# Kernel tuning notes

Measured on AMD Instinct MI355X. Metric: run time of the kernel, lower is better.

Reference implementation:

```python
import jax, jax.numpy as jnp
import numpy as np

N_NODES = 100000
N_EDGES = 3200000  # avg degree 32
IN_FEATS = 512
N_HIDDEN = 128
N_CLASSES = 64
K = 10  # n_layers of gated APPNP propagation


def setup_inputs() -> dict:
    key = jax.random.key(0)
    ks = jax.random.split(key, 6)
    features = jax.random.normal(ks[0], (N_NODES, IN_FEATS), dtype=jnp.float32)
    W1 = jax.random.normal(ks[1], (IN_FEATS, N_HIDDEN), dtype=jnp.float32) * (1.0 / np.sqrt(IN_FEATS))
    b1 = jnp.zeros((N_HIDDEN,), jnp.float32)
    W2 = jax.random.normal(ks[2], (N_HIDDEN, N_CLASSES), dtype=jnp.float32) * (1.0 / np.sqrt(N_HIDDEN))
    b2 = jnp.zeros((N_CLASSES,), jnp.float32)
    init_weight_y = jax.random.normal(ks[3], (IN_FEATS, N_CLASSES), dtype=jnp.float32) * (1.0 / np.sqrt(IN_FEATS))
    edge_index = jax.random.randint(ks[4], (2, N_EDGES), 0, N_NODES, dtype=jnp.int32)
    return {
        "features": features, "W1": W1, "b1": b1, "W2": W2, "b2": b2,
        "init_weight_y": init_weight_y, "edge_index": edge_index,
    }


def reference(features, W1, b1, W2, b2, init_weight_y, edge_index):
    # Eval-mode forward: feat/edge dropout are identity.
    src, dst = edge_index[0], edge_index[1]
    n = features.shape[0]
    # Symmetric GCN normalization D^{-1/2} A D^{-1/2} from in-degrees.
    deg = jax.ops.segment_sum(jnp.ones(src.shape, features.dtype), dst, num_segments=n)
    norm = jax.lax.rsqrt(jnp.clip(deg, 1.0))
    ew = (norm[src] * norm[dst])[:, None]  # [E,1] edge weights

    def spmm(x):  # A_hat @ x via gather-multiply-scatter
        return jax.ops.segment_sum(x[src] * ew, dst, num_segments=n)

    # feature transform: dropout(identity) -> linear -> relu
    h = jax.nn.relu(features @ W1 + b1)                      # [N,H]
    logits = jax.nn.softmax(features @ init_weight_y, axis=1)  # [N,C]
    # project predictions before propagation (APPNP propagates class scores)
    h0 = h @ W2 + b2                                         # [N,C]

    def step(carry, _):
        hc, lg = carry
        agg_lg = spmm(lg)                                    # neighbor soft labels
        # gate: per-node agreement between own and aggregated soft labels
        z = jax.nn.sigmoid(jnp.sum(lg * agg_lg, axis=1, keepdims=True))  # [N,1]
        h_new = z * spmm(hc) + (1.0 - z) * h0                # gated APPNP hop
        return (h_new, agg_lg), None

    (h_out, _), _ = jax.lax.scan(step, (h0, logits), None, length=K)
    return h_out
```

## Files before the change

### kernel.cpp

```cpp
#include <hip/hip_runtime.h>

typedef __attribute__((ext_vector_type(8))) short bf16x8;
typedef __attribute__((ext_vector_type(4))) short bf16x4;
typedef __attribute__((ext_vector_type(4))) float f32x4;
typedef __attribute__((ext_vector_type(4))) unsigned int u32x4;

__device__ __forceinline__ unsigned short f2bf(float f) {
  unsigned int u = __float_as_uint(f);
  u += 0x7fffu + ((u >> 16) & 1u);
  return (unsigned short)(u >> 16);
}
__device__ __forceinline__ float bflo(unsigned int w) { return __uint_as_float(w << 16); }
__device__ __forceinline__ float bfhi(unsigned int w) { return __uint_as_float(w & 0xffff0000u); }

__device__ __forceinline__ unsigned e8(float f) {
  unsigned u = __float_as_uint(f) + (1u << 19);
  int cd = (int)(u >> 20) - 920;
  cd = cd < 0 ? 0 : (cd > 255 ? 255 : cd);
  return (unsigned)cd;
}
__device__ __forceinline__ float d8(unsigned code) {
  return __uint_as_float((code << 20) + (115u << 23));
}

__device__ __forceinline__ short* ldsp(short* base, int row, int rowbytes, int colshort) {
  int off = row * rowbytes + colshort * 2;
  off ^= ((row & 7) << 4);
  return (short*)((char*)base + off);
}

#define CHUNK 8192
#define NBMAX 512
#define BCAP 12288
#define DCAP 96

__global__ __launch_bounds__(256) void k_bucket(const int* __restrict__ ei,
                                                int* __restrict__ gcur,
                                                int2* __restrict__ bpairs, int E, int NB) {
  __shared__ int lhist[NBMAX];
  __shared__ int lbase[NBMAX];
  __shared__ int lcur[NBMAX];
  for (int t = threadIdx.x; t < NB; t += 256) lhist[t] = 0;
  __syncthreads();
  int base = blockIdx.x * CHUNK;
#pragma unroll
  for (int i = 0; i < CHUNK / 256; ++i) {
    int e = base + i * 256 + threadIdx.x;
    if (e < E) atomicAdd(&lhist[ei[E + e] >> 8], 1);
  }
  __syncthreads();
  for (int t = threadIdx.x; t < NB; t += 256) {
    int c = lhist[t];
    lbase[t] = c ? atomicAdd(&gcur[t], c) : 0;
    lcur[t] = 0;
  }
  __syncthreads();
#pragma unroll
  for (int i = 0; i < CHUNK / 256; ++i) {
    int e = base + i * 256 + threadIdx.x;
    if (e < E) {
      int s = ei[e], d = ei[E + e];
      int b = d >> 8;
      int p = lbase[b] + atomicAdd(&lcur[b], 1);
      bpairs[(size_t)b * BCAP + p] = make_int2(s, d);
    }
  }
}

__global__ __launch_bounds__(256) void k_csr(const int2* __restrict__ bpairs,
                                             const int* __restrict__ bcnt,
                                             int* __restrict__ offs, int* __restrict__ deg,
                                             float* __restrict__ nrm,
                                             int* __restrict__ csr_src,
                                             int* __restrict__ gslots, int N) {
  __shared__ int hist[256];
  __shared__ int scan[256];
  __shared__ int cur[256];
  const int t = threadIdx.x;
  const int b = blockIdx.x;
  const int d0 = b << 8;
  const int nn = min(256, N - d0);
  const int base = b * BCAP;
  const int end = base + bcnt[b];
  hist[t] = 0;
  __syncthreads();
  for (int e = base + t; e < end; e += 256) atomicAdd(&hist[bpairs[e].y - d0], 1);
  __syncthreads();
  int myc = hist[t];
  scan[t] = myc;
  __syncthreads();
  for (int o = 1; o < 256; o <<= 1) {
    int x = (t >= o) ? scan[t - o] : 0;
    __syncthreads();
    scan[t] += x;
    __syncthreads();
  }
  int excl = scan[t] - myc;
  if (t < nn) {
    offs[d0 + t] = base + excl;
    deg[d0 + t] = myc;
    nrm[d0 + t] = rsqrtf(fmaxf((float)myc, 1.f));
  }
  if (t < 64) {
    int w0 = hist[4 * t + 0], w1 = hist[4 * t + 1];
    int w2 = hist[4 * t + 2], w3 = hist[4 * t + 3];
    gslots[b * 64 + t] = 4 * max(max(w0, w1), max(w2, w3));
  }
  cur[t] = excl;
  __syncthreads();
  for (int e = base + t; e < end; e += 256) {
    int2 pr = bpairs[e];
    int pos = atomicAdd(&cur[pr.y - d0], 1);
    csr_src[base + pos] = pr.x;
  }
}

__global__ void k_scan1(const int* __restrict__ in, int* __restrict__ out,
                        int* __restrict__ bsum, int n) {
  __shared__ int sm[1024];
  int t = threadIdx.x;
  int gid = blockIdx.x * 1024 + t;
  int v = (gid < n) ? in[gid] : 0;
  sm[t] = v;
  __syncthreads();
  for (int off = 1; off < 1024; off <<= 1) {
    int x = (t >= off) ? sm[t - off] : 0;
    __syncthreads();
    sm[t] += x;
    __syncthreads();
  }
  if (gid < n) out[gid] = sm[t] - v;
  if (t == 1023) bsum[blockIdx.x] = sm[1023];
}

__global__ void k_scan2(int* __restrict__ bsum, int nb) {
  __shared__ int sm[128];
  int t = threadIdx.x;
  int v = (t < nb) ? bsum[t] : 0;
  sm[t] = v;
  __syncthreads();
  for (int o = 1; o < 128; o <<= 1) {
    int x = (t >= o) ? sm[t - o] : 0;
    __syncthreads();
    sm[t] += x;
    __syncthreads();
  }
  if (t < nb) bsum[t] = sm[t] - v;
  if (t == 127) bsum[nb] = sm[127];
}

__global__ void k_scan3(int* __restrict__ out, const int* __restrict__ bsum, int n) {
  int gid = blockIdx.x * 1024 + threadIdx.x;
  if (gid < n) out[gid] += bsum[blockIdx.x];
  if (gid == 0) out[n] = bsum[gridDim.x];
}

__global__ __launch_bounds__(64) void k_ell(
    const int* __restrict__ offs, const int* __restrict__ deg,
    const int* __restrict__ csr_src,
    const int* __restrict__ gof, unsigned* __restrict__ pidx,
    unsigned* __restrict__ HA, unsigned* __restrict__ HB,
    unsigned* __restrict__ LA, unsigned* __restrict__ LB, int N) {
  __shared__ int buf[4][DCAP];
  __shared__ int srt[4][DCAP];
  int g = blockIdx.x;
  int t = threadIdx.x;
  if (g == 0) {
    if (t < 32) { HA[(size_t)N * 32 + t] = 0; HB[(size_t)N * 32 + t] = 0; }
    if (t < 16) { LA[(size_t)N * 16 + t] = 0; LB[(size_t)N * 16 + t] = 0; }
  }
  int base = gof[g];
  int slots = gof[g + 1] - base;
  int o[4], d[4];
#pragma unroll
  for (int s = 0; s < 4; ++s) {
    int nd_ = g * 4 + s;
    o[s] = (nd_ < N) ? offs[nd_] : 0;
    d[s] = (nd_ < N) ? deg[nd_] : 0;
  }
  const int ls = t >> 4;
  const int ll = t & 15;
  const int dd = d[ls];
  const bool srtable = (dd <= DCAP);
  if (srtable)
    for (int i = ll; i < dd; i += 16) buf[ls][i] = csr_src[o[ls] + i];
  __syncthreads();
  if (srtable) {
    for (int i = ll; i < dd; i += 16) {
      int key = buf[ls][i];
      int r = 0;
      for (int j = 0; j < dd; ++j) {
        int v = buf[ls][j];
        r += (v < key) || (v == key && j < i);
      }
      srt[ls][r] = key;
    }
  }
  __syncthreads();
  unsigned zoff = (unsigned)N << 6;
  for (int j = t; j < slots; j += 64) {
    int i = j >> 2, s = j & 3;
    unsigned v = zoff;
    if (i < d[s]) v = (unsigned)((d[s] <= DCAP) ? srt[s][i] : csr_src[o[s] + i]) << 6;
    pidx[base + j] = v;
  }
}

__global__ void k_wprep(const float* __restrict__ W1, const float* __restrict__ Wy,
                        unsigned short* __restrict__ Wt) {
  int k = blockIdx.x, j = threadIdx.x;
  float v = (j < 128) ? W1[k * 128 + j] : Wy[k * 64 + (j - 128)];
  Wt[j * 512 + k] = f2bf(v);
}
__global__ void k_wprep2(const float* __restrict__ W2, unsigned short* __restrict__ Wt2) {
  int k = blockIdx.x, j = threadIdx.x;
  Wt2[j * 128 + k] = f2bf(W2[k * 64 + j]);
}

__global__ __launch_bounds__(256) void k_transform(
    const unsigned short* __restrict__ Wt, const unsigned short* __restrict__ Wt2,
    const float* __restrict__ X, const float* __restrict__ b1, const float* __restrict__ b2,
    const float* __restrict__ nrm,
    unsigned* __restrict__ Hrow0, unsigned* __restrict__ Lrow0,
    unsigned short* __restrict__ h0b, int n)
{
  __shared__ short Xs[128 * 32];
  __shared__ short Ws[192 * 32];
  __shared__ short Hs[128 * 128];
  __shared__ short W2s[64 * 128];

  const int tid = threadIdx.x;
  const int w = tid >> 6;
  const int lane = tid & 63;
  const int c = lane & 15;
  const int g = lane >> 4;
  const int m0 = blockIdx.x * 128;

#pragma unroll
  for (int i = 0; i < 4; ++i) {
    int cc = tid + i * 256;
    int j2 = cc >> 4, k8 = (cc & 15) * 8;
    bf16x8 v = *(const bf16x8*)&Wt2[j2 * 128 + k8];
    *(bf16x8*)ldsp(W2s, j2, 256, k8) = v;
  }

  f32x4 zero4 = {0.f, 0.f, 0.f, 0.f};
  f32x4 acc[2][12];
#pragma unroll
  for (int mi = 0; mi < 2; ++mi)
#pragma unroll
    for (int i = 0; i < 12; ++i) acc[mi][i] = zero4;

  const int xr = tid >> 1;
  const int xc = (tid & 1) * 16;
  const int xrow = m0 + xr;

  for (int kk = 0; kk < 512; kk += 32) {
    float4 f[4];
    if (xrow < n) {
      const float4* p = (const float4*)(X + (size_t)xrow * 512 + kk + xc);
      f[0] = p[0]; f[1] = p[1]; f[2] = p[2]; f[3] = p[3];
    } else {
      float4 z = {0.f, 0.f, 0.f, 0.f};
      f[0] = z; f[1] = z; f[2] = z; f[3] = z;
    }
    {
      const float* fp = (const float*)f;
      unsigned p0, p1, p2, p3, q0, q1, q2, q3;
      asm("v_cvt_pk_bf16_f32 %0, %1, %2" : "=v"(p0) : "v"(fp[0]),  "v"(fp[1]));
      asm("v_cvt_pk_bf16_f32 %0, %1, %2" : "=v"(p1) : "v"(fp[2]),  "v"(fp[3]));
      asm("v_cvt_pk_bf16_f32 %0, %1, %2" : "=v"(p2) : "v"(fp[4]),  "v"(fp[5]));
      asm("v_cvt_pk_bf16_f32 %0, %1, %2" : "=v"(p3) : "v"(fp[6]),  "v"(fp[7]));
      asm("v_cvt_pk_bf16_f32 %0, %1, %2" : "=v"(q0) : "v"(fp[8]),  "v"(fp[9]));
      asm("v_cvt_pk_bf16_f32 %0, %1, %2" : "=v"(q1) : "v"(fp[10]), "v"(fp[11]));
      asm("v_cvt_pk_bf16_f32 %0, %1, %2" : "=v"(q2) : "v"(fp[12]), "v"(fp[13]));
      asm("v_cvt_pk_bf16_f32 %0, %1, %2" : "=v"(q3) : "v"(fp[14]), "v"(fp[15]));
      u32x4 lo = {p0, p1, p2, p3};
      u32x4 hi = {q0, q1, q2, q3};
      *(u32x4*)ldsp(Xs, xr, 64, xc) = lo;
      *(u32x4*)ldsp(Xs, xr, 64, xc + 8) = hi;
    }
#pragma unroll
    for (int i = 0; i < 3; ++i) {
      int cc = tid + i * 256;
      int j = cc >> 2, k8 = (cc & 3) * 8;
      bf16x8 v = *(const bf16x8*)&Wt[j * 512 + kk + k8];
      *(bf16x8*)ldsp(Ws, j, 64, k8) = v;
    }
    __syncthreads();
    bf16x8 bx0 = *(const bf16x8*)ldsp(Xs, w * 32 + c, 64, g * 8);
    bf16x8 bx1 = *(const bf16x8*)ldsp(Xs, w * 32 + 16 + c, 64, g * 8);
#pragma unroll
    for (int jt = 0; jt < 12; ++jt) {
      bf16x8 aw = *(const bf16x8*)ldsp(Ws, jt * 16 + c, 64, g * 8);
      acc[0][jt] = __builtin_amdgcn_mfma_f32_16x16x32_bf16(aw, bx0, acc[0][jt], 0, 0, 0);
      acc[1][jt] = __builtin_amdgcn_mfma_f32_16x16x32_bf16(aw, bx1, acc[1][jt], 0, 0, 0);
    }
    __syncthreads();
  }

  float lv[2][16];
  float inv_[2];
#pragma unroll
  for (int mi = 0; mi < 2; ++mi) {
    int m = w * 32 + mi * 16 + c;
#pragma unroll
    for (int jt = 0; jt < 8; ++jt) {
      int jb = jt * 16 + g * 4;
      bf16x4 hv;
#pragma unroll
      for (int q = 0; q < 4; ++q) {
        float hvf = fmaxf(acc[mi][jt][q] + b1[jb + q], 0.f);
        hv[q] = (short)f2bf(hvf);
      }
      *(bf16x4*)ldsp(Hs, m, 256, jb) = hv;
    }
    float mx = -3.4e38f;
#pragma unroll
    for (int t = 0; t < 4; ++t)
#pragma unroll
      for (int q = 0; q < 4; ++q) {
        float vv = acc[mi][8 + t][q];
        lv[mi][t * 4 + q] = vv;
        mx = fmaxf(mx, vv);
      }
    mx = fmaxf(mx, __shfl_xor(mx, 16, 64));
    mx = fmaxf(mx, __shfl_xor(mx, 32, 64));
    float sum = 0.f;
#pragma unroll
    for (int i = 0; i < 16; ++i) { lv[mi][i] = __expf(lv[mi][i] - mx); sum += lv[mi][i]; }
    sum += __shfl_xor(sum, 16, 64);
    sum += __shfl_xor(sum, 32, 64);
    inv_[mi] = 1.f / sum;
  }
  __syncthreads();

  f32x4 acc2[2][4];
#pragma unroll
  for (int mi = 0; mi < 2; ++mi)
#pragma unroll
    for (int i = 0; i < 4; ++i) acc2[mi][i] = zero4;
#pragma unroll
  for (int kk2 = 0; kk2 < 4; ++kk2) {
    bf16x8 bh0 = *(const bf16x8*)ldsp(Hs, w * 32 + c, 256, kk2 * 32 + g * 8);
    bf16x8 bh1 = *(const bf16x8*)ldsp(Hs, w * 32 + 16 + c, 256, kk2 * 32 + g * 8);
#pragma unroll
    for (int j2t = 0; j2t < 4; ++j2t) {
      bf16x8 a2 = *(const bf16x8*)ldsp(W2s, j2t * 16 + c, 256, kk2 * 32 + g * 8);
      acc2[0][j2t] = __builtin_amdgcn_mfma_f32_16x16x32_bf16(a2, bh0, acc2[0][j2t], 0, 0, 0);
      acc2[1][j2t] = __builtin_amdgcn_mfma_f32_16x16x32_bf16(a2, bh1, acc2[1][j2t], 0, 0, 0);
    }
  }

#pragma unroll
  for (int mi = 0; mi < 2; ++mi) {
    int m = w * 32 + mi * 16 + c;
    int grow = m0 + m;
    if (grow < n) {
      float nd = nrm[grow];
#pragma unroll
      for (int t = 0; t < 4; ++t) {
        int cb = t * 16 + g * 4;
        bf16x4 hb;
        unsigned short hs[4];
        unsigned lw = 0;
#pragma unroll
        for (int q = 0; q < 4; ++q) {
          float lg  = lv[mi][t * 4 + q] * inv_[mi];
          float h0v = acc2[mi][t][q] + b2[cb + q];
          hb[q]  = (short)f2bf(h0v);
          hs[q]  = f2bf(nd * h0v);
          lw |= e8(64.f * nd * lg) << (8 * q);
        }
        uint2 hw;
        hw.x = (unsigned)hs[0] | ((unsigned)hs[1] << 16);
        hw.y = (unsigned)hs[2] | ((unsigned)hs[3] << 16);
        *(uint2*)((char*)Hrow0 + (size_t)grow * 128 + cb * 2) = hw;
        *(unsigned*)((char*)Lrow0 + (size_t)grow * 64 + cb) = lw;
        *(bf16x4*)(h0b + (size_t)grow * 64 + cb) = hb;
      }
    }
  }
}

__global__ __launch_bounds__(256) void k_prop(
    const int* __restrict__ gof, const unsigned* __restrict__ pidx,
    const unsigned* __restrict__ Hin, const unsigned* __restrict__ Lin,
    unsigned* __restrict__ Hout, unsigned* __restrict__ Lout,
    const unsigned short* __restrict__ h0b, const float* __restrict__ nrm,
    float* __restrict__ final_out, int n, int ng, int last)
{
  const int lane = threadIdx.x & 63;
  const int g = blockIdx.x * 4 + (threadIdx.x >> 6);
  if (g >= ng) return;
  const int sub = lane >> 4;
  const int cq  = lane & 15;
  const int node = g * 4 + sub;
  const int beg = gof[g];
  const int w = (gof[g + 1] - beg) >> 2;
  const char* Hc = (const char*)Hin;
  const char* Lc = (const char*)Lin;
  const unsigned* ib = pidx + beg + sub;
  const int hco = cq << 3;
  const int lco = cq << 2;

  const int nodeC = (node < n) ? node : 0;
  unsigned ownl = *(const unsigned*)(Lc + ((size_t)nodeC << 6) + lco);
  float nd = nrm[nodeC];
  bf16x4 h0v = *(const bf16x4*)(h0b + (size_t)nodeC * 64 + cq * 4);

  float aH[4] = {0.f, 0.f, 0.f, 0.f}, aL[4] = {0.f, 0.f, 0.f, 0.f};
  float bH[4] = {0.f, 0.f, 0.f, 0.f}, bL[4] = {0.f, 0.f, 0.f, 0.f};
  int i = 0;
  for (; i + 4 <= w; i += 4) {
    unsigned x0 = ib[4 * i], x1 = ib[4 * i + 4], x2 = ib[4 * i + 8], x3 = ib[4 * i + 12];
    uint2 h0_ = *(const uint2*)(Hc + (((size_t)x0 << 1) + hco));
    uint2 h1_ = *(const uint2*)(Hc + (((size_t)x1 << 1) + hco));
    uint2 h2_ = *(const uint2*)(Hc + (((size_t)x2 << 1) + hco));
    uint2 h3_ = *(const uint2*)(Hc + (((size_t)x3 << 1) + hco));
    unsigned l0 = *(const unsigned*)(Lc + (x0 + lco));
    unsigned l1 = *(const unsigned*)(Lc + (x1 + lco));
    unsigned l2 = *(const unsigned*)(Lc + (x2 + lco));
    unsigned l3 = *(const unsigned*)(Lc + (x3 + lco));
    aH[0] += bflo(h0_.x) + bflo(h2_.x); aH[1] += bfhi(h0_.x) + bfhi(h2_.x);
    aH[2] += bflo(h0_.y) + bflo(h2_.y); aH[3] += bfhi(h0_.y) + bfhi(h2_.y);
    bH[0] += bflo(h1_.x) + bflo(h3_.x); bH[1] += bfhi(h1_.x) + bfhi(h3_.x);
    bH[2] += bflo(h1_.y) + bflo(h3_.y); bH[3] += bfhi(h1_.y) + bfhi(h3_.y);
#pragma unroll
    for (int q = 0; q < 4; ++q) {
      aL[q] += d8((l0 >> (8 * q)) & 255u) + d8((l2 >> (8 * q)) & 255u);
      bL[q] += d8((l1 >> (8 * q)) & 255u) + d8((l3 >> (8 * q)) & 255u);
    }
  }
  for (; i < w; ++i) {
    unsigned x0 = ib[4 * i];
    uint2 h0_ = *(const uint2*)(Hc + (((size_t)x0 << 1) + hco));
    unsigned l0 = *(const unsigned*)(Lc + (x0 + lco));
    aH[0] += bflo(h0_.x); aH[1] += bfhi(h0_.x);
    aH[2] += bflo(h0_.y); aH[3] += bfhi(h0_.y);
#pragma unroll
    for (int q = 0; q < 4; ++q) aL[q] += d8((l0 >> (8 * q)) & 255u);
  }
#pragma unroll
  for (int q = 0; q < 4; ++q) { aH[q] += bH[q]; aL[q] += bL[q]; }

  if (node >= n) return;
  float p = 0.f;
#pragma unroll
  for (int q = 0; q < 4; ++q) p += d8((ownl >> (8 * q)) & 255u) * aL[q];
  p += __shfl_xor(p, 1, 64);
  p += __shfl_xor(p, 2, 64);
  p += __shfl_xor(p, 4, 64);
  p += __shfl_xor(p, 8, 64);
  float z = 1.f / (1.f + __expf(-p * (1.f / 4096.f)));

  if (last) {
    float4 o;
    float* op = &o.x;
#pragma unroll
    for (int q = 0; q < 4; ++q) {
      float h0f = __uint_as_float(((unsigned)(unsigned short)h0v[q]) << 16);
      op[q] = z * nd * aH[q] + (1.f - z) * h0f;
    }
    *(float4*)(final_out + (size_t)node * 64 + cq * 4) = o;
  } else {
    float nn2 = nd * nd;
    unsigned short hs[4];
    unsigned lw = 0;
#pragma unroll
    for (int q = 0; q < 4; ++q) {
      float h0f = __uint_as_float(((unsigned)(unsigned short)h0v[q]) << 16);
      float hn = z * nd * aH[q] + (1.f - z) * h0f;
      hs[q] = f2bf(nd * hn);
      lw |= e8(nn2 * aL[q]) << (8 * q);
    }
    uint2 hw;
    hw.x = (unsigned)hs[0] | ((unsigned)hs[1] << 16);
    hw.y = (unsigned)hs[2] | ((unsigned)hs[3] << 16);
    *(uint2*)((char*)Hout + (((size_t)node << 7) + hco)) = hw;
    *(unsigned*)((char*)Lout + (((size_t)node << 6) + lco)) = lw;
  }
}

extern "C" void kernel_launch(void* const* d_in, const int* in_sizes, int n_in,
                              void* d_out, int out_size, void* d_ws, size_t ws_size,
                              hipStream_t stream) {
  (void)n_in; (void)out_size; (void)ws_size;
  const float* X  = (const float*)d_in[0];
  const float* W1 = (const float*)d_in[1];
  const float* b1 = (const float*)d_in[2];
  const float* W2 = (const float*)d_in[3];
  const float* b2 = (const float*)d_in[4];
  const float* Wy = (const float*)d_in[5];
  const int*   ei = (const int*)d_in[6];
  const int N = in_sizes[0] / 512;
  const int E = in_sizes[6] / 2;
  const int NB = (N + 255) >> 8;
  const int NG = NB * 64;
  const int NWG = (E + CHUNK - 1) / CHUNK;

  char* p = (char*)d_ws;
  auto alloc = [&](size_t bytes) -> char* {
    char* r = p; p += (bytes + 255) & ~(size_t)255; return r;
  };
  int*            gcur    = (int*)  alloc(NBMAX * 4);
  int*            offs    = (int*)  alloc((size_t)N * 4);
  int*            deg     = (int*)  alloc((size_t)N * 4);
  float*          nrm     = (float*)alloc((size_t)N * 4);
  int*            csr_src = (int*)  alloc((size_t)NB * BCAP * 4);
  int*            gslots  = (int*)  alloc((size_t)(NG + 1) * 4);
  int*            gof     = (int*)  alloc((size_t)(NG + 1) * 4);
  int*            sbsum   = (int*)  alloc(1024);
  unsigned*       pidx    = (unsigned*)alloc((size_t)2 * E * 4);
  unsigned short* Wt      = (unsigned short*)alloc(192 * 512 * 2);
  unsigned short* Wt2     = (unsigned short*)alloc(64 * 128 * 2);
  size_t hbytes = (size_t)(N + 1) * 128;
  size_t lbytes = (size_t)(N + 1) * 64;
  size_t bpbytes = (size_t)NB * BCAP * 8;
  char*           shared0 = alloc(bpbytes > hbytes ? bpbytes : hbytes);
  int2*           bpairs  = (int2*)shared0;
  unsigned*       HA      = (unsigned*)shared0;
  unsigned*       HB      = (unsigned*)alloc(hbytes);
  unsigned*       LA      = (unsigned*)alloc(lbytes);
  unsigned*       LB      = (unsigned*)alloc(lbytes);
  unsigned short* h0b     = (unsigned short*)alloc((size_t)N * 64 * 2);

  hipMemsetAsync(gcur, 0, NBMAX * 4, stream);

  k_wprep<<<512, 192, 0, stream>>>(W1, Wy, Wt);
  k_wprep2<<<128, 64, 0, stream>>>(W2, Wt2);
  k_bucket<<<NWG, 256, 0, stream>>>(ei, gcur, bpairs, E, NB);
  k_csr<<<NB, 256, 0, stream>>>(bpairs, gcur, offs, deg, nrm, csr_src, gslots, N);
  int nb2 = (NG + 1023) / 1024;
  k_scan1<<<nb2, 1024, 0, stream>>>(gslots, gof, sbsum, NG);
  k_scan2<<<1, 128, 0, stream>>>(sbsum, nb2);
  k_scan3<<<nb2, 1024, 0, stream>>>(gof, sbsum, NG);
  k_ell<<<NG, 64, 0, stream>>>(offs, deg, csr_src, gof, pidx, HA, HB, LA, LB, N);
  k_transform<<<(N + 127) / 128, 256, 0, stream>>>(Wt, Wt2, X, b1, b2, nrm, HA, LA, h0b, N);

  for (int k = 0; k < 10; ++k) {
    const unsigned* Hin = (k & 1) ? HB : HA;
    unsigned*       Hout = (k & 1) ? HA : HB;
    const unsigned* Lin = (k & 1) ? LB : LA;
    unsigned*       Lout = (k & 1) ? LA : LB;
    k_prop<<<(NG + 3) / 4, 256, 0, stream>>>(gof, pidx, Hin, Lin, Hout, Lout, h0b, nrm,
                                             (float*)d_out, N, NG, (k == 9) ? 1 : 0);
  }
}
```

Before: 1.155 ms.

## Sort nodes by degree within buckets to cut ELL padding in propagation

Within each 256-node bucket, nodes are ranked by in-degree and a nodemap permutation is stored. ELL groups of four nodes are formed from degree-adjacent nodes, so each group's slot count (4× the max degree in the group) wastes less padding, and the ELL build and propagation kernels look up their nodes through the map. The transform kernel also aliases its shared-memory buffers into one 48KB region to lower LDS use and possibly raise occupancy. In exchange there is an O(256) ranking loop per thread in k_csr and an extra indirection per node, and output writes become less coalesced.

```diff
diff --git a/kernel.cpp b/kernel.cpp
--- a/kernel.cpp
+++ b/kernel.cpp
@@ -72,10 +72,12 @@
                                              int* __restrict__ offs, int* __restrict__ deg,
                                              float* __restrict__ nrm,
                                              int* __restrict__ csr_src,
-                                             int* __restrict__ gslots, int N) {
+                                             int* __restrict__ gslots,
+                                             int* __restrict__ nodemap, int N) {
   __shared__ int hist[256];
   __shared__ int scan[256];
   __shared__ int cur[256];
+  __shared__ int dsrt[256];
   const int t = threadIdx.x;
   const int b = blockIdx.x;
   const int d0 = b << 8;
@@ -101,13 +103,16 @@
     deg[d0 + t] = myc;
     nrm[d0 + t] = rsqrtf(fmaxf((float)myc, 1.f));
   }
-  if (t < 64) {
-    int w0 = hist[4 * t + 0], w1 = hist[4 * t + 1];
-    int w2 = hist[4 * t + 2], w3 = hist[4 * t + 3];
-    gslots[b * 64 + t] = 4 * max(max(w0, w1), max(w2, w3));
-  }
   cur[t] = excl;
-  __syncthreads();
+  int r = 0;
+  for (int j = 0; j < 256; ++j) {
+    int dj = hist[j];
+    r += (dj < myc) || (dj == myc && j < t);
+  }
+  dsrt[r] = myc;
+  nodemap[d0 + r] = d0 + t;
+  __syncthreads();
+  if (t < 64) gslots[b * 64 + t] = 4 * dsrt[4 * t + 3];
   for (int e = base + t; e < end; e += 256) {
     int2 pr = bpairs[e];
     int pos = atomicAdd(&cur[pr.y - d0], 1);
@@ -158,7 +163,8 @@
 __global__ __launch_bounds__(64) void k_ell(
     const int* __restrict__ offs, const int* __restrict__ deg,
     const int* __restrict__ csr_src,
-    const int* __restrict__ gof, unsigned* __restrict__ pidx,
+    const int* __restrict__ gof, const int* __restrict__ nodemap,
+    unsigned* __restrict__ pidx,
     unsigned* __restrict__ HA, unsigned* __restrict__ HB,
     unsigned* __restrict__ LA, unsigned* __restrict__ LB, int N) {
   __shared__ int buf[4][DCAP];
@@ -174,9 +180,9 @@
   int o[4], d[4];
 #pragma unroll
   for (int s = 0; s < 4; ++s) {
-    int nd_ = g * 4 + s;
-    o[s] = (nd_ < N) ? offs[nd_] : 0;
-    d[s] = (nd_ < N) ? deg[nd_] : 0;
+    int node = nodemap[g * 4 + s];
+    o[s] = (node < N) ? offs[node] : 0;
+    d[s] = (node < N) ? deg[node] : 0;
   }
   const int ls = t >> 4;
   const int ll = t & 15;
@@ -224,10 +230,11 @@
     unsigned* __restrict__ Hrow0, unsigned* __restrict__ Lrow0,
     unsigned short* __restrict__ h0b, int n)
 {
-  __shared__ short Xs[128 * 32];
-  __shared__ short Ws[192 * 32];
-  __shared__ short Hs[128 * 128];
-  __shared__ short W2s[64 * 128];
+  __shared__ __align__(16) char smem[49152];
+  short* Xs  = (short*)smem;
+  short* Ws  = (short*)(smem + 8192);
+  short* Hs  = (short*)smem;
+  short* W2s = (short*)(smem + 32768);
 
   const int tid = threadIdx.x;
   const int w = tid >> 6;
@@ -384,7 +391,8 @@
 }
 
 __global__ __launch_bounds__(256) void k_prop(
-    const int* __restrict__ gof, const unsigned* __restrict__ pidx,
+    const int* __restrict__ gof, const int* __restrict__ nodemap,
+    const unsigned* __restrict__ pidx,
     const unsigned* __restrict__ Hin, const unsigned* __restrict__ Lin,
     unsigned* __restrict__ Hout, unsigned* __restrict__ Lout,
     const unsigned short* __restrict__ h0b, const float* __restrict__ nrm,
@@ -395,7 +403,7 @@
   if (g >= ng) return;
   const int sub = lane >> 4;
   const int cq  = lane & 15;
-  const int node = g * 4 + sub;
+  const int node = nodemap[g * 4 + sub];
   const int beg = gof[g];
   const int w = (gof[g + 1] - beg) >> 2;
   const char* Hc = (const char*)Hin;
@@ -507,6 +515,7 @@
   int*            offs    = (int*)  alloc((size_t)N * 4);
   int*            deg     = (int*)  alloc((size_t)N * 4);
   float*          nrm     = (float*)alloc((size_t)N * 4);
+  int*            nodemap = (int*)  alloc((size_t)NB * 256 * 4);
   int*            csr_src = (int*)  alloc((size_t)NB * BCAP * 4);
   int*            gslots  = (int*)  alloc((size_t)(NG + 1) * 4);
   int*            gof     = (int*)  alloc((size_t)(NG + 1) * 4);
@@ -530,12 +539,12 @@
   k_wprep<<<512, 192, 0, stream>>>(W1, Wy, Wt);
   k_wprep2<<<128, 64, 0, stream>>>(W2, Wt2);
   k_bucket<<<NWG, 256, 0, stream>>>(ei, gcur, bpairs, E, NB);
-  k_csr<<<NB, 256, 0, stream>>>(bpairs, gcur, offs, deg, nrm, csr_src, gslots, N);
+  k_csr<<<NB, 256, 0, stream>>>(bpairs, gcur, offs, deg, nrm, csr_src, gslots, nodemap, N);
   int nb2 = (NG + 1023) / 1024;
   k_scan1<<<nb2, 1024, 0, stream>>>(gslots, gof, sbsum, NG);
   k_scan2<<<1, 128, 0, stream>>>(sbsum, nb2);
   k_scan3<<<nb2, 1024, 0, stream>>>(gof, sbsum, NG);
-  k_ell<<<NG, 64, 0, stream>>>(offs, deg, csr_src, gof, pidx, HA, HB, LA, LB, N);
+  k_ell<<<NG, 64, 0, stream>>>(offs, deg, csr_src, gof, nodemap, pidx, HA, HB, LA, LB, N);
   k_transform<<<(N + 127) / 128, 256, 0, stream>>>(Wt, Wt2, X, b1, b2, nrm, HA, LA, h0b, N);
 
   for (int k = 0; k < 10; ++k) {
@@ -543,7 +552,7 @@
     unsigned*       Hout = (k & 1) ? HA : HB;
     const unsigned* Lin = (k & 1) ? LB : LA;
     unsigned*       Lout = (k & 1) ? LA : LB;
-    k_prop<<<(NG + 3) / 4, 256, 0, stream>>>(gof, pidx, Hin, Lin, Hout, Lout, h0b, nrm,
-                                             (float*)d_out, N, NG, (k == 9) ? 1 : 0);
-  }
-}
+    k_prop<<<(NG + 3) / 4, 256, 0, stream>>>(gof, nodemap, pidx, Hin, Lin, Hout, Lout,
+                                             h0b, nrm, (float*)d_out, N, NG, (k == 9) ? 1 : 0);
+  }
+}
```

Result: slower. 1.277 ms (+10.5%).
